# Optimization experiments

Measured on AMD Instinct MI355X. Metric: run time of the kernel, lower is better.

The kernel has to match this reference:

```python
import jax, jax.numpy as jnp
import numpy as np

B, S, D, H = 2, 2048, 1024, 16
DK = D // H

def setup_inputs() -> dict:
    key = jax.random.key(0)
    ks = jax.random.split(key, 5)
    scale = 1.0 / np.sqrt(D)
    return {
        "query": jax.random.normal(ks[0], (B, S, D), dtype=jnp.float32),
        "mask": jnp.ones((B, S, S), dtype=jnp.int32),
        "Wq": jax.random.normal(ks[1], (D, D), dtype=jnp.float32) * scale,
        "bq": jnp.zeros((D,), dtype=jnp.float32),
        "Wk": jax.random.normal(ks[2], (D, D), dtype=jnp.float32) * scale,
        "bk": jnp.zeros((D,), dtype=jnp.float32),
        "Wv": jax.random.normal(ks[3], (D, D), dtype=jnp.float32) * scale,
        "bv": jnp.zeros((D,), dtype=jnp.float32),
        "Wo": jax.random.normal(ks[4], (D, D), dtype=jnp.float32) * scale,
        "bo": jnp.zeros((D,), dtype=jnp.float32),
    }

def reference(query, mask, Wq, bq, Wk, bk, Wv, bv, Wo, bo):
    # self-attention: key = value = query (torch Linear: x @ W.T + b)
    b, s, d = query.shape
    def proj(x, W, bias):
        y = jnp.einsum('bsd,ed->bse', x, W) + bias
        return y.reshape(b, s, H, DK).transpose(0, 2, 1, 3)  # [B,H,S,DK]
    q = proj(query, Wq, bq)
    k = proj(query, Wk, bk)
    v = proj(query, Wv, bv)
    scores = jnp.einsum('bhqd,bhkd->bhqk', q, k) / jnp.sqrt(jnp.float32(DK))
    m = mask[:, None, :, :]  # [B,1,S,S] (torch unsqueeze(1) for 3D mask)
    scores = jnp.where(m == 0, jnp.float32(-1e9), scores)
    w = jax.nn.softmax(scores, axis=-1)  # dropout: eval mode -> identity
    o = jnp.einsum('bhqk,bhkd->bhqd', w, v)
    o = o.transpose(0, 2, 1, 3).reshape(b, s, d)
    return jnp.einsum('bsd,ed->bse', o, Wo) + bo
```

## Files before the change

kernel.cpp:

```cpp
#include <hip/hip_runtime.h>


typedef _Float16 f16x8 __attribute__((ext_vector_type(8)));
typedef _Float16 f16x4 __attribute__((ext_vector_type(4)));
typedef _Float16 f16x2 __attribute__((ext_vector_type(2)));
typedef float    f32x4 __attribute__((ext_vector_type(4)));
typedef float    f32x16 __attribute__((ext_vector_type(16)));
typedef int      i32x4 __attribute__((ext_vector_type(4)));

#define MFMA32(a, b, c) __builtin_amdgcn_mfma_f32_32x32x16_f16(a, b, c, 0, 0, 0)
#define MFMA16(a, b, c) __builtin_amdgcn_mfma_f32_16x16x32_f16(a, b, c, 0, 0, 0)

__device__ __forceinline__ void gld16(const void* g, void* l) {
    __builtin_amdgcn_global_load_lds(
        (const __attribute__((address_space(1))) void*)g,
        (__attribute__((address_space(3))) void*)l, 16, 0, 0);
}

__device__ __forceinline__ void conv1k(const float* __restrict__ in,
                                       _Float16* __restrict__ out, int base) {
    const int i = base + threadIdx.x * 4;
    float4 v = *(const float4*)(in + i);
    f16x4 o;
    o.x = (_Float16)v.x; o.y = (_Float16)v.y; o.z = (_Float16)v.z; o.w = (_Float16)v.w;
    *(f16x4*)(out + i) = o;
}

__global__ void k_pre(const float* __restrict__ X, const float* __restrict__ Wq,
                      const float* __restrict__ Wk, const float* __restrict__ Wv,
                      const float* __restrict__ Wo,
                      _Float16* __restrict__ Xh, _Float16* __restrict__ Wqh,
                      _Float16* __restrict__ Wkh, _Float16* __restrict__ Wvh,
                      _Float16* __restrict__ Woh,
                      const int* __restrict__ mask, int* __restrict__ flag) {
    const int bid = blockIdx.x;
    if (bid < 4096)      conv1k(X,  Xh,  bid * 1024);
    else if (bid < 5120) conv1k(Wq, Wqh, (bid - 4096) * 1024);
    else if (bid < 6144) conv1k(Wk, Wkh, (bid - 5120) * 1024);
    else if (bid < 7168) conv1k(Wv, Wvh, (bid - 6144) * 1024);
    else if (bid < 8192) conv1k(Wo, Woh, (bid - 7168) * 1024);
    else {
        const int i = (bid - 8192) * 1024 + threadIdx.x * 4;
        int4 v = *(const int4*)(mask + i);
        if ((v.x == 0) | (v.y == 0) | (v.z == 0) | (v.w == 0)) atomicOr(flag, 1);
    }
}

__global__ __launch_bounds__(256, 3) void k_qkv(
    const _Float16* __restrict__ X,
    const _Float16* __restrict__ Wqh, const _Float16* __restrict__ Wkh,
    const _Float16* __restrict__ Wvh,
    const float* __restrict__ bq, const float* __restrict__ bk,
    const float* __restrict__ bv,
    _Float16* __restrict__ Qo, _Float16* __restrict__ Ko, _Float16* __restrict__ Vo)
{
    __shared__ _Float16 SH[128 * 136];
    _Float16* As = SH;
    _Float16* Bs = SH + 128 * 64;
    const int tid = threadIdx.x;
    const int lane = tid & 63, wv = tid >> 6;
    const int wrow = wv >> 1, wcol = wv & 1;
    const int l5 = lane & 31, half = lane >> 5;
    const int which = blockIdx.x >> 3;
    const _Float16* W   = which == 0 ? Wqh : which == 1 ? Wkh : Wvh;
    const float*   bias = which == 0 ? bq  : which == 1 ? bk  : bv;
    const int n0 = (blockIdx.x & 7) * 128;
    const int m0 = blockIdx.y * 128;

    f32x16 acc[2][2];
#pragma unroll
    for (int a = 0; a < 2; ++a)
#pragma unroll
        for (int bb = 0; bb < 2; ++bb)
#pragma unroll
            for (int r = 0; r < 16; ++r) acc[a][bb][r] = 0.f;

#pragma unroll 1
    for (int k0 = 0; k0 < 1024; k0 += 64) {
        __syncthreads();
#pragma unroll
        for (int it = 0; it < 4; ++it) {
            const int wbase = it * 256 + wv * 64;
            const int ci = wbase + lane;
            const int r = ci >> 3;
            const int c8 = (((ci & 7) ^ (r & 7)) * 8);
            gld16(X + (size_t)(m0 + r) * 1024 + k0 + c8, As + wbase * 8);
            gld16(W + (size_t)(n0 + r) * 1024 + k0 + c8, Bs + wbase * 8);
        }
        __syncthreads();
#pragma unroll
        for (int ks = 0; ks < 4; ++ks) {
            f16x8 af[2], bf[2];
#pragma unroll
            for (int mt = 0; mt < 2; ++mt)
                af[mt] = *(const f16x8*)(As + (wrow * 64 + mt * 32 + l5) * 64 +
                                         (((ks * 2 + half) ^ (l5 & 7)) * 8));
#pragma unroll
            for (int nt = 0; nt < 2; ++nt)
                bf[nt] = *(const f16x8*)(Bs + (wcol * 64 + nt * 32 + l5) * 64 +
                                         (((ks * 2 + half) ^ (l5 & 7)) * 8));
#pragma unroll
            for (int mt = 0; mt < 2; ++mt)
#pragma unroll
                for (int nt = 0; nt < 2; ++nt)
                    acc[mt][nt] = MFMA32(af[mt], bf[nt], acc[mt][nt]);
        }
    }

    __syncthreads();
    const int b_ = m0 >> 11;
    const int s_base = m0 & 2047;
    if (which == 2) {
#pragma unroll
        for (int nt = 0; nt < 2; ++nt) {
            const int e_l = wcol * 64 + nt * 32 + l5;
            const float bv_ = bias[n0 + e_l];
#pragma unroll
            for (int mt = 0; mt < 2; ++mt)
#pragma unroll
                for (int g = 0; g < 4; ++g) {
                    const int m_l = wrow * 64 + mt * 32 + 8 * g + 4 * half;
                    f16x4 pk;
#pragma unroll
                    for (int j = 0; j < 4; ++j)
                        pk[j] = (_Float16)(acc[mt][nt][4 * g + j] + bv_);
                    *(f16x4*)(SH + e_l * 136 + m_l) = pk;
                }
        }
        __syncthreads();
#pragma unroll
        for (int p = 0; p < 8; ++p) {
            const int e_l = p * 16 + (tid >> 4);
            const int s8 = (tid & 15) * 8;
            f16x8 vv = *(const f16x8*)(SH + e_l * 136 + s8);
            const int e = n0 + e_l;
            const int h = e >> 6, dk = e & 63;
            *(f16x8*)(Vo + (((size_t)b_ * 16 + h) * 64 + dk) * 2048 + s_base + s8) = vv;
        }
    } else {
        const float qs = (which == 0) ? 0.18033688011112042f : 1.0f;
        _Float16* Out = which == 0 ? Qo : Ko;
#pragma unroll
        for (int nt = 0; nt < 2; ++nt) {
            const int e_l = wcol * 64 + nt * 32 + l5;
            const float bv_ = bias[n0 + e_l];
#pragma unroll
            for (int mt = 0; mt < 2; ++mt)
#pragma unroll
                for (int r = 0; r < 16; ++r) {
                    const int m_l = wrow * 64 + mt * 32 + (r & 3) + 8 * (r >> 2) + 4 * half;
                    SH[m_l * 136 + e_l] = (_Float16)((acc[mt][nt][r] + bv_) * qs);
                }
        }
        __syncthreads();
#pragma unroll
        for (int p = 0; p < 8; ++p) {
            const int m_l = p * 16 + (tid >> 4);
            const int c8 = (tid & 15) * 8;
            f16x8 vv = *(const f16x8*)(SH + m_l * 136 + c8);
            const int e = n0 + c8;
            const int h = e >> 6, dk = e & 63;
            const int s = s_base + m_l;
            *(f16x8*)(Out + (((size_t)b_ * 16 + h) * 2048 + s) * 64 + dk) = vv;
        }
    }
}

__global__ __launch_bounds__(256, 4) void k_oproj(
    const _Float16* __restrict__ Oin, const _Float16* __restrict__ Woh,
    const float* __restrict__ bo, float* __restrict__ out)
{
    __shared__ _Float16 As[128 * 64];
    __shared__ _Float16 Bs[64 * 64];
    const int tid = threadIdx.x;
    const int lane = tid & 63, wv = tid >> 6;
    const int quad = lane >> 4, lc = lane & 15;
    const int n0 = blockIdx.x * 64;
    const int m0 = blockIdx.y * 128;

    const f32x4 fzero = {0.f, 0.f, 0.f, 0.f};
    f32x4 acc[2][4];
#pragma unroll
    for (int a = 0; a < 2; ++a)
#pragma unroll
        for (int bb = 0; bb < 4; ++bb) acc[a][bb] = fzero;

#pragma unroll 1
    for (int k0 = 0; k0 < 1024; k0 += 64) {
        __syncthreads();
#pragma unroll
        for (int it = 0; it < 4; ++it) {
            const int ci = it * 256 + tid;
            const int r = ci >> 3;
            const int c8 = (((ci & 7) ^ (r & 7)) * 8);
            gld16(Oin + (size_t)(m0 + r) * 1024 + k0 + c8, As + ci * 8);
        }
#pragma unroll
        for (int it = 0; it < 2; ++it) {
            const int ci = it * 256 + tid;
            const int r = ci >> 3;
            const int c8 = (((ci & 7) ^ (r & 7)) * 8);
            gld16(Woh + (size_t)(n0 + r) * 1024 + k0 + c8, Bs + ci * 8);
        }
        __syncthreads();
#pragma unroll
        for (int ks = 0; ks < 2; ++ks) {
            f16x8 af[2], bf[4];
#pragma unroll
            for (int mt = 0; mt < 2; ++mt)
                af[mt] = *(const f16x8*)(As + (wv * 32 + mt * 16 + lc) * 64 +
                                         (((ks * 4 + quad) ^ (lc & 7)) * 8));
#pragma unroll
            for (int nt = 0; nt < 4; ++nt)
                bf[nt] = *(const f16x8*)(Bs + (nt * 16 + lc) * 64 +
                                         (((ks * 4 + quad) ^ (lc & 7)) * 8));
#pragma unroll
            for (int mt = 0; mt < 2; ++mt)
#pragma unroll
                for (int nt = 0; nt < 4; ++nt)
                    acc[mt][nt] = MFMA16(af[mt], bf[nt], acc[mt][nt]);
        }
    }
#pragma unroll
    for (int nt = 0; nt < 4; ++nt) {
        const int e = n0 + nt * 16 + lc;
        const float bv_ = bo[e];
#pragma unroll
        for (int mt = 0; mt < 2; ++mt)
#pragma unroll
            for (int i = 0; i < 4; ++i) {
                const int m = m0 + wv * 32 + mt * 16 + quad * 4 + i;
                out[(size_t)m * 1024 + e] = acc[mt][nt][i] + bv_;
            }
    }
}

__global__ __launch_bounds__(512, 4) void k_attn(
    const _Float16* __restrict__ Q, const _Float16* __restrict__ K,
    const _Float16* __restrict__ Vt, const int* __restrict__ mask,
    const int* __restrict__ flag, _Float16* __restrict__ O)
{
    __shared__ __align__(16) char SMEM[66560];
    _Float16* Ks = (_Float16*)SMEM;
    _Float16* Vs = (_Float16*)(SMEM + 32768);
    float*    Os = (float*)SMEM;
    float*    Ls = (float*)(SMEM + 65536);

    const int tid = threadIdx.x;
    const int lane = tid & 63, wv = tid >> 6;
    const int l5 = lane & 31, half = lane >> 5;
    const int bh = blockIdx.y;
    const int b = bh >> 4, h = bh & 15;
    const int qb = blockIdx.x * 32;

    const _Float16* Qb = Q  + (size_t)bh * 2048 * 64;
    const _Float16* Kb = K  + (size_t)bh * 2048 * 64;
    const _Float16* Vb = Vt + (size_t)bh * 64 * 2048;

    f16x8 qf[4];
#pragma unroll
    for (int kk = 0; kk < 4; ++kk)
        qf[kk] = *(const f16x8*)(Qb + (size_t)(qb + l5) * 64 + kk * 16 + half * 8);

    f32x16 o[2];
#pragma unroll
    for (int nt = 0; nt < 2; ++nt)
#pragma unroll
        for (int r = 0; r < 16; ++r) o[nt][r] = 0.f;
    float l_i = 0.f;

    const bool has_zero = (*flag != 0);
    const int swl = (l5 & 7) ^ ((l5 >> 3) & 3);

#pragma unroll 1
    for (int kt = 0; kt < 8; ++kt) {
        const int k0 = kt * 256;
        __syncthreads();
#pragma unroll
        for (int it = 0; it < 4; ++it) {
            const int p = it * 512 + tid;
            const int r = p >> 3;
            const int c = (p & 7) ^ (r & 7) ^ ((r >> 3) & 3);
            gld16(Kb + (size_t)(k0 + r) * 64 + c * 8, Ks + p * 8);
            const int dk = p >> 5;
            const int cv = (p & 31) ^ (dk & 31);
            gld16(Vb + (size_t)dk * 2048 + k0 + cv * 8, Vs + p * 8);
        }
        __syncthreads();

        f32x16 st;
#pragma unroll
        for (int r = 0; r < 16; ++r) st[r] = 0.f;
#pragma unroll
        for (int kk = 0; kk < 4; ++kk) {
            const int row = wv * 32 + l5;
            f16x8 kf = *(const f16x8*)(Ks + row * 64 + (((kk * 2 + half) ^ swl) * 8));
            st = MFMA32(kf, qf[kk], st);
        }

        if (has_zero) {
            const int q = qb + l5;
            const int* mr = mask + ((size_t)b * 2048 + q) * 2048 + k0 + wv * 32;
            for (int r = 0; r < 16; ++r) {
                const int kk_ = (r & 3) + 8 * (r >> 2) + 4 * half;
                if (mr[kk_] == 0) st[r] = -1e30f;
            }
        }

        float rs = 0.f;
#pragma unroll
        for (int r = 0; r < 16; ++r) {
            const float p = exp2f(st[r]);
            st[r] = p;
            rs += p;
        }
        rs += __shfl_xor(rs, 32);
        l_i += rs;

        int u[8], s[8];
#pragma unroll
        for (int j = 0; j < 8; ++j)
            u[j] = __builtin_bit_cast(int,
                       __builtin_amdgcn_cvt_pkrtz(st[2 * j], st[2 * j + 1]));
#pragma unroll
        for (int j = 0; j < 8; ++j) s[j] = __shfl_xor(u[j], 32);
        i32x4 a0 = { half ? s[2] : u[0], half ? s[3] : u[1],
                     half ? u[2] : s[0], half ? u[3] : s[1] };
        i32x4 a1 = { half ? s[6] : u[4], half ? s[7] : u[5],
                     half ? u[6] : s[4], half ? u[7] : s[5] };
        f16x8 pa0 = __builtin_bit_cast(f16x8, a0);
        f16x8 pa1 = __builtin_bit_cast(f16x8, a1);

#pragma unroll
        for (int nt = 0; nt < 2; ++nt) {
            const int dk = nt * 32 + l5;
            f16x8 vf0 = *(const f16x8*)(Vs + dk * 256 +
                            (((wv * 4 + 0 * 2 + half) ^ (dk & 31)) * 8));
            f16x8 vf1 = *(const f16x8*)(Vs + dk * 256 +
                            (((wv * 4 + 1 * 2 + half) ^ (dk & 31)) * 8));
            o[nt] = MFMA32(pa0, vf0, o[nt]);
            o[nt] = MFMA32(pa1, vf1, o[nt]);
        }
    }

    __syncthreads();
    if (half == 0) Ls[wv * 32 + l5] = l_i;
    {
        float* Ob = Os + wv * 2048;
#pragma unroll
        for (int nt = 0; nt < 2; ++nt)
#pragma unroll
            for (int r = 0; r < 16; ++r) {
                const int q_loc = (r & 3) + 8 * (r >> 2) + 4 * half;
                Ob[q_loc * 64 + nt * 32 + l5] = o[nt][r];
            }
    }
    __syncthreads();
    {
        const int q_loc = tid >> 4;
        const int dg = (tid & 15) * 4;
        f32x4 acc = {0.f, 0.f, 0.f, 0.f};
        float lt = 0.f;
#pragma unroll
        for (int w = 0; w < 8; ++w) {
            acc += *(const f32x4*)(Os + w * 2048 + q_loc * 64 + dg);
            lt += Ls[w * 32 + q_loc];
        }
        const float linv = 1.f / lt;
        f16x4 ov;
#pragma unroll
        for (int j = 0; j < 4; ++j) ov[j] = (_Float16)(acc[j] * linv);
        const int q = qb + q_loc;
        *(f16x4*)(O + ((size_t)b * 2048 + q) * 1024 + h * 64 + dg) = ov;
    }
}

extern "C" void kernel_launch(void* const* d_in, const int* in_sizes, int n_in,
                              void* d_out, int out_size, void* d_ws, size_t ws_size,
                              hipStream_t stream) {
    const float* query = (const float*)d_in[0];
    const int*   mask  = (const int*)d_in[1];
    const float* Wq = (const float*)d_in[2]; const float* bq = (const float*)d_in[3];
    const float* Wk = (const float*)d_in[4]; const float* bk = (const float*)d_in[5];
    const float* Wv = (const float*)d_in[6]; const float* bv = (const float*)d_in[7];
    const float* Wo = (const float*)d_in[8]; const float* bo = (const float*)d_in[9];
    float* out = (float*)d_out;

    char* ws = (char*)d_ws;
    _Float16* Xh  = (_Float16*)(ws);
    _Float16* Wqh = (_Float16*)(ws + 8388608);
    _Float16* Wkh = (_Float16*)(ws + 10485760);
    _Float16* Wvh = (_Float16*)(ws + 12582912);
    _Float16* Woh = (_Float16*)(ws + 14680064);
    _Float16* Qh  = (_Float16*)(ws + 16777216);
    _Float16* Kh  = (_Float16*)(ws + 25165824);
    _Float16* Vh  = (_Float16*)(ws + 33554432);
    _Float16* Oh  = Xh;
    int* flag     = (int*)(ws + 41943040);

    (void)hipMemsetAsync(flag, 0, 4, stream);
    k_pre<<<16384, 256, 0, stream>>>(query, Wq, Wk, Wv, Wo,
                                     Xh, Wqh, Wkh, Wvh, Woh, mask, flag);
    k_qkv<<<dim3(24, 32), 256, 0, stream>>>(Xh, Wqh, Wkh, Wvh, bq, bk, bv, Qh, Kh, Vh);
    k_attn<<<dim3(64, 32), 512, 0, stream>>>(Qh, Kh, Vh, mask, flag, Oh);
    k_oproj<<<dim3(16, 32), 256, 0, stream>>>(Oh, Woh, bo, out);
}
```

Baseline: 244.3 us.

## Pre-swizzle K/V into MFMA fragment layout and load directly from global memory

The QKV projection now writes K and V in a layout already packed per MFMA fragment, so the attention kernel can read each lane's operand with one contiguous 16-byte global load and no LDS staging. Attention work is repartitioned so each wave owns 32 queries and scans all keys, in 256-thread blocks. This removes the cross-wave LDS reduction of partial outputs and the per-tile barriers. In exchange it depends on L2/cache reuse of K/V across waves and has less latency hiding with no explicit prefetch. The final output store becomes scalar f16 writes.

```diff
diff --git a/kernel.cpp b/kernel.cpp
--- a/kernel.cpp
+++ b/kernel.cpp
@@ -3,7 +3,6 @@
 
 typedef _Float16 f16x8 __attribute__((ext_vector_type(8)));
 typedef _Float16 f16x4 __attribute__((ext_vector_type(4)));
-typedef _Float16 f16x2 __attribute__((ext_vector_type(2)));
 typedef float    f32x4 __attribute__((ext_vector_type(4)));
 typedef float    f32x16 __attribute__((ext_vector_type(16)));
 typedef int      i32x4 __attribute__((ext_vector_type(4)));
@@ -135,11 +134,13 @@
             f16x8 vv = *(const f16x8*)(SH + e_l * 136 + s8);
             const int e = n0 + e_l;
             const int h = e >> 6, dk = e & 63;
-            *(f16x8*)(Vo + (((size_t)b_ * 16 + h) * 64 + dk) * 2048 + s_base + s8) = vv;
+            const int s0 = s_base + s8;
+            const size_t idx = ((((size_t)(b_ * 16 + h) * 128 + (s0 >> 4)) * 2 +
+                                (dk >> 5)) * 64 + (dk & 31) + 32 * ((s8 >> 3) & 1)) * 8;
+            *(f16x8*)(Vo + idx) = vv;
         }
     } else {
         const float qs = (which == 0) ? 0.18033688011112042f : 1.0f;
-        _Float16* Out = which == 0 ? Qo : Ko;
 #pragma unroll
         for (int nt = 0; nt < 2; ++nt) {
             const int e_l = wcol * 64 + nt * 32 + l5;
@@ -161,7 +162,13 @@
             const int e = n0 + c8;
             const int h = e >> 6, dk = e & 63;
             const int s = s_base + m_l;
-            *(f16x8*)(Out + (((size_t)b_ * 16 + h) * 2048 + s) * 64 + dk) = vv;
+            if (which == 0) {
+                *(f16x8*)(Qo + (((size_t)b_ * 16 + h) * 2048 + s) * 64 + dk) = vv;
+            } else {
+                const size_t idx = ((((size_t)(b_ * 16 + h) * 64 + (s >> 5)) * 4 +
+                                    (dk >> 4)) * 64 + (s & 31) + 32 * ((dk >> 3) & 1)) * 8;
+                *(f16x8*)(Ko + idx) = vv;
+            }
         }
     }
 }
@@ -235,27 +242,21 @@
     }
 }
 
-__global__ __launch_bounds__(512, 4) void k_attn(
-    const _Float16* __restrict__ Q, const _Float16* __restrict__ K,
-    const _Float16* __restrict__ Vt, const int* __restrict__ mask,
+__global__ __launch_bounds__(256, 2) void k_attn(
+    const _Float16* __restrict__ Q, const _Float16* __restrict__ Kp,
+    const _Float16* __restrict__ Vp, const int* __restrict__ mask,
     const int* __restrict__ flag, _Float16* __restrict__ O)
 {
-    __shared__ __align__(16) char SMEM[66560];
-    _Float16* Ks = (_Float16*)SMEM;
-    _Float16* Vs = (_Float16*)(SMEM + 32768);
-    float*    Os = (float*)SMEM;
-    float*    Ls = (float*)(SMEM + 65536);
-
     const int tid = threadIdx.x;
     const int lane = tid & 63, wv = tid >> 6;
     const int l5 = lane & 31, half = lane >> 5;
     const int bh = blockIdx.y;
     const int b = bh >> 4, h = bh & 15;
-    const int qb = blockIdx.x * 32;
+    const int qb = blockIdx.x * 128 + wv * 32;
 
     const _Float16* Qb = Q  + (size_t)bh * 2048 * 64;
-    const _Float16* Kb = K  + (size_t)bh * 2048 * 64;
-    const _Float16* Vb = Vt + (size_t)bh * 64 * 2048;
+    const _Float16* Kb = Kp + (size_t)bh * 131072;
+    const _Float16* Vb = Vp + (size_t)bh * 131072;
 
     f16x8 qf[4];
 #pragma unroll
@@ -270,37 +271,30 @@
     float l_i = 0.f;
 
     const bool has_zero = (*flag != 0);
-    const int swl = (l5 & 7) ^ ((l5 >> 3) & 3);
-
-#pragma unroll 1
-    for (int kt = 0; kt < 8; ++kt) {
-        const int k0 = kt * 256;
-        __syncthreads();
-#pragma unroll
-        for (int it = 0; it < 4; ++it) {
-            const int p = it * 512 + tid;
-            const int r = p >> 3;
-            const int c = (p & 7) ^ (r & 7) ^ ((r >> 3) & 3);
-            gld16(Kb + (size_t)(k0 + r) * 64 + c * 8, Ks + p * 8);
-            const int dk = p >> 5;
-            const int cv = (p & 31) ^ (dk & 31);
-            gld16(Vb + (size_t)dk * 2048 + k0 + cv * 8, Vs + p * 8);
-        }
-        __syncthreads();
+
+#pragma unroll 2
+    for (int kb = 0; kb < 64; ++kb) {
+        f16x8 kf[4];
+#pragma unroll
+        for (int kk = 0; kk < 4; ++kk)
+            kf[kk] = *(const f16x8*)(Kb + ((size_t)(kb * 4 + kk) * 64 + lane) * 8);
+        f16x8 vf[4];
+#pragma unroll
+        for (int ks = 0; ks < 2; ++ks)
+#pragma unroll
+            for (int nt = 0; nt < 2; ++nt)
+                vf[ks * 2 + nt] = *(const f16x8*)(Vb +
+                    ((size_t)((kb * 2 + ks) * 2 + nt) * 64 + lane) * 8);
 
         f32x16 st;
 #pragma unroll
         for (int r = 0; r < 16; ++r) st[r] = 0.f;
 #pragma unroll
-        for (int kk = 0; kk < 4; ++kk) {
-            const int row = wv * 32 + l5;
-            f16x8 kf = *(const f16x8*)(Ks + row * 64 + (((kk * 2 + half) ^ swl) * 8));
-            st = MFMA32(kf, qf[kk], st);
-        }
+        for (int kk = 0; kk < 4; ++kk) st = MFMA32(kf[kk], qf[kk], st);
 
         if (has_zero) {
             const int q = qb + l5;
-            const int* mr = mask + ((size_t)b * 2048 + q) * 2048 + k0 + wv * 32;
+            const int* mr = mask + ((size_t)b * 2048 + q) * 2048 + kb * 32;
             for (int r = 0; r < 16; ++r) {
                 const int kk_ = (r & 3) + 8 * (r >> 2) + 4 * half;
                 if (mr[kk_] == 0) st[r] = -1e30f;
@@ -331,47 +325,22 @@
         f16x8 pa0 = __builtin_bit_cast(f16x8, a0);
         f16x8 pa1 = __builtin_bit_cast(f16x8, a1);
 
-#pragma unroll
-        for (int nt = 0; nt < 2; ++nt) {
-            const int dk = nt * 32 + l5;
-            f16x8 vf0 = *(const f16x8*)(Vs + dk * 256 +
-                            (((wv * 4 + 0 * 2 + half) ^ (dk & 31)) * 8));
-            f16x8 vf1 = *(const f16x8*)(Vs + dk * 256 +
-                            (((wv * 4 + 1 * 2 + half) ^ (dk & 31)) * 8));
-            o[nt] = MFMA32(pa0, vf0, o[nt]);
-            o[nt] = MFMA32(pa1, vf1, o[nt]);
-        }
-    }
-
-    __syncthreads();
-    if (half == 0) Ls[wv * 32 + l5] = l_i;
-    {
-        float* Ob = Os + wv * 2048;
+        o[0] = MFMA32(pa0, vf[0], o[0]);
+        o[1] = MFMA32(pa0, vf[1], o[1]);
+        o[0] = MFMA32(pa1, vf[2], o[0]);
+        o[1] = MFMA32(pa1, vf[3], o[1]);
+    }
+
+    const float linv = 1.f / l_i;
+#pragma unroll
+    for (int r = 0; r < 16; ++r) {
+        const int q_loc = (r & 3) + 8 * (r >> 2) + 4 * half;
+        const float lv = __shfl(linv, q_loc);
+        const int q = qb + q_loc;
+        _Float16* orow = O + ((size_t)b * 2048 + q) * 1024 + h * 64;
 #pragma unroll
         for (int nt = 0; nt < 2; ++nt)
-#pragma unroll
-            for (int r = 0; r < 16; ++r) {
-                const int q_loc = (r & 3) + 8 * (r >> 2) + 4 * half;
-                Ob[q_loc * 64 + nt * 32 + l5] = o[nt][r];
-            }
-    }
-    __syncthreads();
-    {
-        const int q_loc = tid >> 4;
-        const int dg = (tid & 15) * 4;
-        f32x4 acc = {0.f, 0.f, 0.f, 0.f};
-        float lt = 0.f;
-#pragma unroll
-        for (int w = 0; w < 8; ++w) {
-            acc += *(const f32x4*)(Os + w * 2048 + q_loc * 64 + dg);
-            lt += Ls[w * 32 + q_loc];
-        }
-        const float linv = 1.f / lt;
-        f16x4 ov;
-#pragma unroll
-        for (int j = 0; j < 4; ++j) ov[j] = (_Float16)(acc[j] * linv);
-        const int q = qb + q_loc;
-        *(f16x4*)(O + ((size_t)b * 2048 + q) * 1024 + h * 64 + dg) = ov;
+            orow[nt * 32 + l5] = (_Float16)(o[nt][r] * lv);
     }
 }
 
@@ -402,6 +371,6 @@
     k_pre<<<16384, 256, 0, stream>>>(query, Wq, Wk, Wv, Wo,
                                      Xh, Wqh, Wkh, Wvh, Woh, mask, flag);
     k_qkv<<<dim3(24, 32), 256, 0, stream>>>(Xh, Wqh, Wkh, Wvh, bq, bk, bv, Qh, Kh, Vh);
-    k_attn<<<dim3(64, 32), 512, 0, stream>>>(Qh, Kh, Vh, mask, flag, Oh);
+    k_attn<<<dim3(16, 32), 256, 0, stream>>>(Qh, Kh, Vh, mask, flag, Oh);
     k_oproj<<<dim3(16, 32), 256, 0, stream>>>(Oh, Woh, bo, out);
 }
```

Result: faster. 237.2 us (-2.9%).
